# Kernel tuning notes

Hardware: AMD Instinct MI355X
Metric: run time of the kernel (lower is better)

Reference implementation:

```python
import jax, jax.numpy as jnp
import numpy as np

B, L, T = 32, 512, 400
EMB, PRE, ENC, ARNN, DRNN, NSYM = 512, 256, 512, 1024, 1024, 256
MEAN_COEFF, SCALE_COEFF = 1.0, 10.0


def setup_inputs() -> dict:
    key = jax.random.key(0)
    ks = jax.random.split(key, 20)
    s = 0.02
    inp = {
        'memory': jax.random.normal(ks[0], (B, L, ENC), jnp.float32),
        'decoder_inputs': jax.random.normal(ks[1], (B, EMB, T), jnp.float32),
        'memory_lengths': jax.random.randint(ks[2], (B,), L // 2, L + 1).astype(jnp.int64),
        # prenet
        'pW1': jax.random.normal(ks[3], (PRE, EMB), jnp.float32) * s,
        'pb1': jnp.zeros((PRE,), jnp.float32),
        'pW2': jax.random.normal(ks[4], (PRE, PRE), jnp.float32) * s,
        'pb2': jnp.zeros((PRE,), jnp.float32),
        # attention LSTMCell
        'aWih': jax.random.normal(ks[5], (4 * ARNN, PRE + ENC), jnp.float32) * s,
        'aWhh': jax.random.normal(ks[6], (4 * ARNN, ARNN), jnp.float32) * s,
        'abih': jnp.zeros((4 * ARNN,), jnp.float32),
        'abhh': jnp.zeros((4 * ARNN,), jnp.float32),
        # Gaussian attention param linear (weight zero-init in torch; small here)
        'attWp': jax.random.normal(ks[7], (2, ARNN), jnp.float32) * 0.001,
        'attbp': jnp.zeros((2,), jnp.float32),
        # decoder LSTMCell
        'dWih': jax.random.normal(ks[8], (4 * DRNN, ARNN + ENC), jnp.float32) * s,
        'dWhh': jax.random.normal(ks[9], (4 * DRNN, DRNN), jnp.float32) * s,
        'dbih': jnp.zeros((4 * DRNN,), jnp.float32),
        'dbhh': jnp.zeros((4 * DRNN,), jnp.float32),
        # output linear
        'oW': jax.random.normal(ks[10], (NSYM, DRNN + ENC), jnp.float32) * s,
        'ob': jnp.zeros((NSYM,), jnp.float32),
    }
    return inp


def _lstm_cell(x, h, c, Wih, Whh, bih, bhh):
    g = x @ Wih.T + bih + h @ Whh.T + bhh
    i, f, gg, o = jnp.split(g, 4, axis=-1)
    c = jax.nn.sigmoid(f) * c + jax.nn.sigmoid(i) * jnp.tanh(gg)
    h = jax.nn.sigmoid(o) * jnp.tanh(c)
    return h, c


def _decoder_core(memory, decoder_inputs, memory_lengths,
                  pW1, pb1, pW2, pb2,
                  aWih, aWhh, abih, abhh,
                  attWp, attbp,
                  dWih, dWhh, dbih, dbhh,
                  oW, ob):
    b = memory.shape[0]
    Lm = memory.shape[1]
    # go frame + time-major inputs -> prenet (dropout is identity in eval)
    x = jnp.transpose(decoder_inputs, (2, 0, 1))            # [T, B, EMB]
    x = jnp.concatenate([jnp.zeros((1, b, EMB), x.dtype), x], axis=0)  # [T+1, B, EMB]
    x = jax.nn.relu(x @ pW1.T + pb1)
    x = jax.nn.relu(x @ pW2.T + pb2)                        # [T+1, B, PRE]
    x = x[:T]                                               # loop runs T steps

    lin = jnp.arange(Lm, dtype=memory.dtype)[None, :]       # [1, L]
    pad_mask = lin >= memory_lengths[:, None].astype(memory.dtype)  # [B, L] True at pad

    def step(carry, x_t):
        ah, ac, dh, dc, ctx, mean = carry
        cell_in = jnp.concatenate([x_t, ctx], axis=1)
        ah, ac = _lstm_cell(cell_in, ah, ac, aWih, aWhh, abih, abhh)
        params = ah @ attWp.T + attbp                       # [B, 2]
        mean = mean + jnp.exp(params[:, 0:1]) * MEAN_COEFF  # [B, 1]
        scale = jnp.exp(params[:, 1:2]) * SCALE_COEFF       # [B, 1]
        Z = jnp.sqrt(2.0 * np.pi * scale ** 2)
        w = jnp.exp(-0.5 * (lin - mean) ** 2 / scale ** 2) / Z  # [B, L]
        w = jnp.where(pad_mask, 0.0, w)
        ctx = jnp.einsum('bl,bld->bd', w, memory)           # [B, ENC]
        dec_in = jnp.concatenate([ah, ctx], axis=1)
        dh, dc = _lstm_cell(dec_in, dh, dc, dWih, dWhh, dbih, dbhh)
        out = jnp.concatenate([dh, ctx], axis=1) @ oW.T + ob  # [B, NSYM]
        return (ah, ac, dh, dc, ctx, mean), (out, w, params)

    z = jnp.zeros
    carry0 = (z((b, ARNN)), z((b, ARNN)), z((b, DRNN)), z((b, DRNN)),
              z((b, ENC)), z((b, 1)))
    _, (logits, aligns, ps) = jax.lax.scan(step, carry0, x)
    # time-major -> [B, T, ...]
    return (jnp.transpose(logits, (1, 0, 2)),
            jnp.transpose(aligns, (1, 0, 2)),
            jnp.transpose(ps, (1, 0, 2)))


def reference(memory, decoder_inputs, memory_lengths,
              pW1, pb1, pW2, pb2,
              aWih, aWhh, abih, abhh,
              attWp, attbp,
              dWih, dWhh, dbih, dbhh,
              oW, ob):
    return _decoder_core(memory, decoder_inputs, memory_lengths,
                         pW1, pb1, pW2, pb2,
                         aWih, aWhh, abih, abhh,
                         attWp, attbp,
                         dWih, dWhh, dbih, dbhh,
                         oW, ob)
```

## Files before the change

### kernel.cpp

```cpp
#include <hip/hip_runtime.h>
#include <math.h>

#define Bsz   32
#define Lmem  512
#define Tsteps 400
#define EMBD  512
#define PRE   256
#define ENCD  512
#define ARNN  1024
#define DRNN  1024
#define NSYM  256

typedef _Float16 f16x8 __attribute__((ext_vector_type(8)));
typedef float    f32x4 __attribute__((ext_vector_type(4)));
typedef _Float16 half_t;

#define KA  (PRE + ENCD + ARNN)
#define KAQ (KA / 4)
#define NMA (KAQ / 32)
#define KD  (ARNN + ENCD + DRNN)
#define KDQ (KD / 4)
#define NMD (KDQ / 32)
#define LDA_A 1800
#define LDA_D 2568

__device__ __forceinline__ void st_agent_f16(half_t* p, half_t v) {
    __hip_atomic_store((unsigned short*)p, __builtin_bit_cast(unsigned short, v),
                       __ATOMIC_RELAXED, __HIP_MEMORY_SCOPE_AGENT);
}
__device__ __forceinline__ void st_agent_f32(float* p, float v) {
    __hip_atomic_store(p, v, __ATOMIC_RELAXED, __HIP_MEMORY_SCOPE_AGENT);
}
__device__ __forceinline__ void st_agent_u32(unsigned* p, unsigned v) {
    __hip_atomic_store(p, v, __ATOMIC_RELAXED, __HIP_MEMORY_SCOPE_AGENT);
}
__device__ __forceinline__ float ld_agent_f32(const float* p) {
    return __hip_atomic_load(p, __ATOMIC_RELAXED, __HIP_MEMORY_SCOPE_AGENT);
}
__device__ __forceinline__ unsigned ld_agent_u32(const unsigned* p) {
    return __hip_atomic_load(p, __ATOMIC_RELAXED, __HIP_MEMORY_SCOPE_AGENT);
}
__device__ __forceinline__ f16x8 ld_agent_f16x8(const half_t* p) {
    union { unsigned long long u[2]; f16x8 v; } c;
    c.u[0] = __hip_atomic_load((const unsigned long long*)p,
                               __ATOMIC_RELAXED, __HIP_MEMORY_SCOPE_AGENT);
    c.u[1] = __hip_atomic_load(((const unsigned long long*)p) + 1,
                               __ATOMIC_RELAXED, __HIP_MEMORY_SCOPE_AGENT);
    return c.v;
}

template<int KIH, int KHH>
__global__ __launch_bounds__(256) void conv_lstm_w(
    const float* __restrict__ Wih, const float* __restrict__ Whh,
    const float* __restrict__ bih, const float* __restrict__ bhh,
    half_t* __restrict__ Wcat, float* __restrict__ bsum)
{
    constexpr int K = KIH + KHH;
    const int j = blockIdx.x;
    const float* srcA = Wih + (size_t)j * KIH;
    const float* srcB = Whh + (size_t)j * KHH;
    half_t* dst = Wcat + (size_t)j * K;
    for (int k = threadIdx.x; k < KIH; k += 256) dst[k]       = (half_t)srcA[k];
    for (int k = threadIdx.x; k < KHH; k += 256) dst[KIH + k] = (half_t)srcB[k];
    if (threadIdx.x == 0) bsum[j] = bih[j] + bhh[j];
}

__global__ __launch_bounds__(256) void conv_mat(
    const float* __restrict__ src, half_t* __restrict__ dst, int n)
{
    for (int i = blockIdx.x * 256 + threadIdx.x; i < n; i += gridDim.x * 256)
        dst[i] = (half_t)src[i];
}

__global__ __launch_bounds__(256) void prenet_kernel(
    const float* __restrict__ din,
    const float* __restrict__ pW1, const float* __restrict__ pb1,
    const float* __restrict__ pW2, const float* __restrict__ pb2,
    half_t* __restrict__ xpre)
{
    __shared__ float xs[8][EMBD];
    __shared__ float h1s[8][PRE];
    const int tid = threadIdx.x;
    const int row0 = blockIdx.x * 8;

    for (int idx = tid; idx < 8 * EMBD; idx += 256) {
        int r = idx >> 9;
        int e = idx & 511;
        int rid = row0 + r;
        int t = rid >> 5;
        int b = rid & 31;
        float v = 0.f;
        if (t > 0) v = din[(size_t)b * EMBD * Tsteps + (size_t)e * Tsteps + (t - 1)];
        xs[r][e] = v;
    }
    __syncthreads();

    {
        float acc[8] = {0.f,0.f,0.f,0.f,0.f,0.f,0.f,0.f};
        const float* wr = pW1 + (size_t)tid * EMBD;
        for (int e = 0; e < EMBD; e += 4) {
            float4 wv = *(const float4*)(wr + e);
            #pragma unroll
            for (int r = 0; r < 8; ++r) {
                float4 xv = *(const float4*)&xs[r][e];
                acc[r] += wv.x * xv.x + wv.y * xv.y + wv.z * xv.z + wv.w * xv.w;
            }
        }
        float bias = pb1[tid];
        #pragma unroll
        for (int r = 0; r < 8; ++r) h1s[r][tid] = fmaxf(acc[r] + bias, 0.f);
    }
    __syncthreads();

    {
        float acc[8] = {0.f,0.f,0.f,0.f,0.f,0.f,0.f,0.f};
        const float* wr = pW2 + (size_t)tid * PRE;
        for (int e = 0; e < PRE; e += 4) {
            float4 wv = *(const float4*)(wr + e);
            #pragma unroll
            for (int r = 0; r < 8; ++r) {
                float4 xv = *(const float4*)&h1s[r][e];
                acc[r] += wv.x * xv.x + wv.y * xv.y + wv.z * xv.z + wv.w * xv.w;
            }
        }
        float bias = pb2[tid];
        #pragma unroll
        for (int r = 0; r < 8; ++r) {
            int rid = row0 + r;
            int t = rid >> 5;
            int b = rid & 31;
            xpre[(size_t)t * Bsz * PRE + (size_t)b * PRE + tid] =
                (half_t)fmaxf(acc[r] + bias, 0.f);
        }
    }
}

__device__ __forceinline__ void gsync(unsigned* flags, unsigned ph)
{
    asm volatile("s_waitcnt vmcnt(0)" ::: "memory");
    __syncthreads();
    if (threadIdx.x == 0)
        __hip_atomic_store(flags + blockIdx.x * 16, ph,
                           __ATOMIC_RELAXED, __HIP_MEMORY_SCOPE_AGENT);
    if (threadIdx.x < 64) {
        const unsigned* f = flags + threadIdx.x * 64;
        for (;;) {
            unsigned a = ld_agent_u32(f);
            unsigned b = ld_agent_u32(f + 16);
            unsigned c = ld_agent_u32(f + 32);
            unsigned d = ld_agent_u32(f + 48);
            unsigned m = min(min(a, b), min(c, d));
            if (m >= ph) break;
            __builtin_amdgcn_s_sleep(2);
        }
    }
    __syncthreads();
}

__global__ __launch_bounds__(512, 1) void decoder_persistent(
    const half_t* __restrict__ Wcat_a, const float* __restrict__ bsum_a,
    const half_t* __restrict__ Wcat_d, const float* __restrict__ bsum_d,
    const half_t* __restrict__ Wo, const float* __restrict__ ob,
    const half_t* __restrict__ xpre,
    const float* __restrict__ attWp, const float* __restrict__ attbp,
    const int* __restrict__ mlen, const half_t* __restrict__ mem16,
    half_t* __restrict__ ah0, half_t* __restrict__ ah1,
    half_t* __restrict__ dh0, half_t* __restrict__ dh1,
    half_t* __restrict__ ctx0, half_t* __restrict__ ctx1,
    float* __restrict__ mean0, float* __restrict__ mean1,
    float* __restrict__ logits, float* __restrict__ aligns,
    float* __restrict__ ps,
    unsigned* flags)
{
    const int blk   = blockIdx.x;
    const int tid   = threadIdx.x;
    const int wave  = tid >> 6;
    const int lane  = tid & 63;
    const int btile = wave & 1;
    const int kq    = wave >> 1;
    const int m15   = lane & 15;
    const int kh    = lane >> 4;
    const int u0    = blk << 2;
    const int bb    = (btile << 4) + m15;

    __shared__ __align__(16) half_t wAl[16 * LDA_A];
    __shared__ __align__(16) half_t wDl[16 * LDA_D];
    __shared__ float gred[4][2][16][16];
    __shared__ float wsh[Lmem];
    __shared__ float lred[16][33];
    __shared__ float wred8[8][2];
    __shared__ float bc2[2];

    for (int g = tid; g < 16 * (KA / 8); g += 512) {
        int r = g / (KA / 8);
        int c = (g - r * (KA / 8)) * 8;
        int jr = (r >> 2) * 1024 + u0 + (r & 3);
        *(f16x8*)(wAl + r * LDA_A + c) = *(const f16x8*)(Wcat_a + (size_t)jr * KA + c);
    }
    for (int g = tid; g < 16 * (KD / 8); g += 512) {
        int r = g / (KD / 8);
        int c = (g - r * (KD / 8)) * 8;
        int jr = (r >> 2) * 1024 + u0 + (r & 3);
        *(f16x8*)(wDl + r * LDA_D + c) = *(const f16x8*)(Wcat_d + (size_t)jr * KD + c);
    }
    float bsA[4] = {0.f,0.f,0.f,0.f}, bsD[4] = {0.f,0.f,0.f,0.f};
    float cA = 0.f, cD = 0.f;
    if (tid < 128) {
        const int ul = tid >> 5;
        #pragma unroll
        for (int gi = 0; gi < 4; ++gi) {
            bsA[gi] = bsum_a[gi * 1024 + u0 + ul];
            bsD[gi] = bsum_d[gi * 1024 + u0 + ul];
        }
    }
    const half_t* lA = wAl + m15 * LDA_A + kq * KAQ + (kh << 3);
    const half_t* lD = wDl + m15 * LDA_D + kq * KDQ + (kh << 3);
    __syncthreads();

    unsigned ph = 0;

    for (int t = 0; t <= Tsteps; ++t) {
        const int par = t & 1;
        half_t*       ah_cur  = par ? ah1 : ah0;
        const half_t* ah_prv  = par ? ah0 : ah1;
        half_t*       ctx_cur = par ? ctx1 : ctx0;
        const half_t* ctx_prv = par ? ctx0 : ctx1;
        float*        mn_cur  = par ? mean1 : mean0;
        const float*  mn_prv  = par ? mean0 : mean1;
        half_t*       dh_s    = par ? dh0 : dh1;
        const half_t* dh_prv  = par ? dh1 : dh0;

        {
            f16x8 bvA[NMA];
            f16x8 bvD[NMD];
            if (t < Tsteps) {
                const half_t* s0 = xpre + (size_t)t * Bsz * PRE;
                #pragma unroll
                for (int i = 0; i < NMA; ++i) {
                    const int kg = kq * KAQ + i * 32 + (kh << 3);
                    const half_t* bp = (kg < PRE)        ? (s0 + bb * PRE + kg)
                                     : (kg < PRE + ENCD) ? (ctx_prv + bb * ENCD + (kg - PRE))
                                                         : (ah_prv + bb * ARNN + (kg - PRE - ENCD));
                    bvA[i] = ld_agent_f16x8(bp);
                }
            }
            if (t > 0) {
                #pragma unroll
                for (int i = 0; i < NMD; ++i) {
                    const int kg = kq * KDQ + i * 32 + (kh << 3);
                    const half_t* bp = (kg < ARNN)        ? (ah_prv + bb * ARNN + kg)
                                     : (kg < ARNN + ENCD) ? (ctx_prv + bb * ENCD + (kg - ARNN))
                                                          : (dh_prv + bb * DRNN + (kg - ARNN - ENCD));
                    bvD[i] = ld_agent_f16x8(bp);
                }
            }
            if (t < Tsteps) {
                f32x4 accA = {0.f,0.f,0.f,0.f};
                #pragma unroll
                for (int i = 0; i < NMA; ++i) {
                    f16x8 av = *(const f16x8*)(lA + i * 32);
                    accA = __builtin_amdgcn_mfma_f32_16x16x32_f16(av, bvA[i], accA, 0, 0, 0);
                }
                #pragma unroll
                for (int r = 0; r < 4; ++r)
                    gred[kq][btile][(kh << 2) + r][m15] = accA[r];
                __syncthreads();
                if (tid < 128) {
                    const int ul = tid >> 5;
                    const int bq = tid & 31;
                    const int bt = bq >> 4;
                    const int nn = bq & 15;
                    float g[4];
                    #pragma unroll
                    for (int gi = 0; gi < 4; ++gi) {
                        const int mr = (gi << 2) + ul;
                        g[gi] = gred[0][bt][mr][nn] + gred[1][bt][mr][nn]
                              + gred[2][bt][mr][nn] + gred[3][bt][mr][nn] + bsA[gi];
                    }
                    float si = 1.f / (1.f + expf(-g[0]));
                    float sf = 1.f / (1.f + expf(-g[1]));
                    float so = 1.f / (1.f + expf(-g[3]));
                    cA = sf * cA + si * tanhf(g[2]);
                    st_agent_f16(&ah_cur[bq * 1024 + u0 + ul], (half_t)(so * tanhf(cA)));
                }
                __syncthreads();
            }
            if (t > 0) {
                f32x4 accD = {0.f,0.f,0.f,0.f};
                #pragma unroll
                for (int i = 0; i < NMD; ++i) {
                    f16x8 av = *(const f16x8*)(lD + i * 32);
                    accD = __builtin_amdgcn_mfma_f32_16x16x32_f16(av, bvD[i], accD, 0, 0, 0);
                }
                #pragma unroll
                for (int r = 0; r < 4; ++r)
                    gred[kq][btile][(kh << 2) + r][m15] = accD[r];
                __syncthreads();
                if (tid < 128) {
                    const int ul = tid >> 5;
                    const int bq = tid & 31;
                    const int bt = bq >> 4;
                    const int nn = bq & 15;
                    float g[4];
                    #pragma unroll
                    for (int gi = 0; gi < 4; ++gi) {
                        const int mr = (gi << 2) + ul;
                        g[gi] = gred[0][bt][mr][nn] + gred[1][bt][mr][nn]
                              + gred[2][bt][mr][nn] + gred[3][bt][mr][nn] + bsD[gi];
                    }
                    float si = 1.f / (1.f + expf(-g[0]));
                    float sf = 1.f / (1.f + expf(-g[1]));
                    float so = 1.f / (1.f + expf(-g[3]));
                    cD = sf * cD + si * tanhf(g[2]);
                    st_agent_f16(&dh_s[bq * 1024 + u0 + ul], (half_t)(so * tanhf(cD)));
                }
            }
        }
        ++ph; gsync(flags, ph);

        if (t < Tsteps) {
            const int abt = blk >> 3;
            const int dt  = blk & 7;
            float p0, p1;
            {
                union { unsigned u; _Float16 h[2]; } a;
                a.u = ld_agent_u32((const unsigned*)(ah_cur + abt * ARNN + 2 * tid));
                float a0 = (float)a.h[0], a1 = (float)a.h[1];
                float2 w0 = *(const float2*)(attWp + 2 * tid);
                float2 w1 = *(const float2*)(attWp + ARNN + 2 * tid);
                p0 = a0 * w0.x + a1 * w0.y;
                p1 = a0 * w1.x + a1 * w1.y;
            }
            #pragma unroll
            for (int off = 32; off > 0; off >>= 1) {
                p0 += __shfl_down(p0, off, 64);
                p1 += __shfl_down(p1, off, 64);
            }
            if (lane == 0) { wred8[wave][0] = p0; wred8[wave][1] = p1; }
            __syncthreads();
            if (tid == 0) {
                float q0 = attbp[0], q1 = attbp[1];
                #pragma unroll
                for (int w = 0; w < 8; ++w) { q0 += wred8[w][0]; q1 += wred8[w][1]; }
                float mn = ld_agent_f32(&mn_prv[abt]) + expf(q0) * 1.0f;
                float sc = expf(q1) * 10.0f;
                if (dt == 0) {
                    st_agent_f32(&mn_cur[abt], mn);
                    st_agent_f32(&ps[(size_t)abt * Tsteps * 2 + (size_t)t * 2 + 0], q0);
                    st_agent_f32(&ps[(size_t)abt * Tsteps * 2 + (size_t)t * 2 + 1], q1);
                }
                bc2[0] = mn; bc2[1] = sc;
            }
            __syncthreads();
            const float mn = bc2[0], sc = bc2[1];
            const float inv_s = 1.f / sc;
            const float coef = 0.3989422804014327f * inv_s;
            const int len = mlen[abt];
            {
                float z = ((float)tid - mn) * inv_s;
                float wv = (tid < len) ? expf(-0.5f * z * z) * coef : 0.f;
                wsh[tid] = wv;
                if (dt == 0)
                    st_agent_f32(&aligns[(size_t)abt * Tsteps * Lmem + (size_t)t * Lmem + tid], wv);
            }
            __syncthreads();
            int lo = (int)fmaxf(0.f, floorf(mn - 9.f * sc));
            int hi = (int)fminf((float)len, ceilf(mn + 9.f * sc) + 1.f);
            const int d8 = (dt << 6) + (wave << 3);
            const half_t* mb = mem16 + (size_t)abt * Lmem * ENCD + d8;
            float acc[8] = {0.f,0.f,0.f,0.f,0.f,0.f,0.f,0.f};
            for (int l = lo + lane; l < hi; l += 64) {
                f16x8 mv = *(const f16x8*)(mb + (size_t)l * ENCD);
                float w = wsh[l];
                #pragma unroll
                for (int j = 0; j < 8; ++j) acc[j] += w * (float)mv[j];
            }
            #pragma unroll
            for (int off = 32; off > 0; off >>= 1) {
                #pragma unroll
                for (int j = 0; j < 8; ++j) acc[j] += __shfl_down(acc[j], off, 64);
            }
            if (lane == 0) {
                #pragma unroll
                for (int j = 0; j < 4; ++j) {
                    union { unsigned u; _Float16 h[2]; } pk;
                    pk.h[0] = (_Float16)acc[2 * j];
                    pk.h[1] = (_Float16)acc[2 * j + 1];
                    st_agent_u32((unsigned*)(ctx_cur + abt * ENCD + d8 + 2 * j), pk.u);
                }
            }
        }
        if (t > 0) {
            const int b_o = tid & 31;
            const int ks  = tid >> 5;
            const half_t* wrow = Wo + (size_t)blk * (DRNN + ENCD) + ks * 96;
            f16x8 wv[12], av[12];
            #pragma unroll
            for (int c8 = 0; c8 < 12; ++c8) {
                const int k = ks * 96 + c8 * 8;
                wv[c8] = *(const f16x8*)(wrow + c8 * 8);
                const half_t* ap = (k < DRNN) ? (dh_s + b_o * DRNN + k)
                                              : (ctx_prv + b_o * ENCD + (k - DRNN));
                av[c8] = ld_agent_f16x8(ap);
            }
            float outacc = 0.f;
            #pragma unroll
            for (int c8 = 0; c8 < 12; ++c8)
                #pragma unroll
                for (int e = 0; e < 8; ++e)
                    outacc += (float)wv[c8][e] * (float)av[c8][e];
            lred[ks][b_o] = outacc;
            __syncthreads();
            if (tid < 32) {
                float s = 0.f;
                #pragma unroll
                for (int q = 0; q < 16; ++q) s += lred[q][tid];
                st_agent_f32(&logits[(size_t)tid * Tsteps * NSYM + (size_t)(t - 1) * NSYM + blk],
                             s + ob[blk]);
            }
        }
        if (t < Tsteps) { ++ph; gsync(flags, ph); }
    }
}

extern "C" void kernel_launch(void* const* d_in, const int* in_sizes, int n_in,
                              void* d_out, int out_size, void* d_ws, size_t ws_size,
                              hipStream_t stream)
{
    (void)in_sizes; (void)n_in; (void)out_size; (void)ws_size;
    const float* memory = (const float*)d_in[0];
    const float* din    = (const float*)d_in[1];
    const int*   mlen   = (const int*)d_in[2];
    const float* pW1    = (const float*)d_in[3];
    const float* pb1    = (const float*)d_in[4];
    const float* pW2    = (const float*)d_in[5];
    const float* pb2    = (const float*)d_in[6];
    const float* aWih   = (const float*)d_in[7];
    const float* aWhh   = (const float*)d_in[8];
    const float* abih   = (const float*)d_in[9];
    const float* abhh   = (const float*)d_in[10];
    const float* attWp  = (const float*)d_in[11];
    const float* attbp  = (const float*)d_in[12];
    const float* dWih   = (const float*)d_in[13];
    const float* dWhh   = (const float*)d_in[14];
    const float* dbih   = (const float*)d_in[15];
    const float* dbhh   = (const float*)d_in[16];
    const float* oW     = (const float*)d_in[17];
    const float* ob     = (const float*)d_in[18];

    float* logits = (float*)d_out;
    float* aligns = logits + (size_t)Bsz * Tsteps * NSYM;
    float* ps     = aligns + (size_t)Bsz * Tsteps * Lmem;

    char* base = (char*)d_ws;
    auto alloc = [&](size_t bytes) -> char* {
        char* p = base; base += (bytes + 255) & ~(size_t)255; return p;
    };
    half_t* Wcat_a = (half_t*)alloc((size_t)4096 * KA * 2);
    half_t* Wcat_d = (half_t*)alloc((size_t)4096 * KD * 2);
    half_t* Wo     = (half_t*)alloc((size_t)NSYM * (DRNN + ENCD) * 2);
    float*  bsum_a = (float*)alloc(4096 * 4);
    float*  bsum_d = (float*)alloc(4096 * 4);
    half_t* xpre   = (half_t*)alloc((size_t)Tsteps * Bsz * PRE * 2);
    half_t* mem16  = (half_t*)alloc((size_t)Bsz * Lmem * ENCD * 2);
    half_t* ah0    = (half_t*)alloc(Bsz * ARNN * 2);
    half_t* ah1    = (half_t*)alloc(Bsz * ARNN * 2);
    half_t* dh0    = (half_t*)alloc(Bsz * DRNN * 2);
    half_t* dh1    = (half_t*)alloc(Bsz * DRNN * 2);
    half_t* ctx0   = (half_t*)alloc(Bsz * ENCD * 2);
    half_t* ctx1   = (half_t*)alloc(Bsz * ENCD * 2);
    float*  mean0  = (float*)alloc(Bsz * 4);
    float*  mean1  = (float*)alloc(Bsz * 4);
    unsigned* flags = (unsigned*)alloc(256 * 16 * 4);

    (void)hipMemsetAsync(ah1,   0, Bsz * ARNN * 2, stream);
    (void)hipMemsetAsync(dh1,   0, Bsz * DRNN * 2, stream);
    (void)hipMemsetAsync(ctx1,  0, Bsz * ENCD * 2, stream);
    (void)hipMemsetAsync(mean0, 0, Bsz * 4, stream);
    (void)hipMemsetAsync(mean1, 0, Bsz * 4, stream);
    (void)hipMemsetAsync(flags, 0, 256 * 16 * 4, stream);

    conv_lstm_w<PRE + ENCD, ARNN><<<4096, 256, 0, stream>>>(
        aWih, aWhh, abih, abhh, Wcat_a, bsum_a);
    conv_lstm_w<ARNN + ENCD, DRNN><<<4096, 256, 0, stream>>>(
        dWih, dWhh, dbih, dbhh, Wcat_d, bsum_d);
    conv_mat<<<768, 256, 0, stream>>>(oW, Wo, NSYM * (DRNN + ENCD));
    conv_mat<<<4096, 256, 0, stream>>>(memory, mem16, Bsz * Lmem * ENCD);
    prenet_kernel<<<Tsteps * Bsz / 8, 256, 0, stream>>>(din, pW1, pb1, pW2, pb2, xpre);

    decoder_persistent<<<256, 512, 0, stream>>>(
        Wcat_a, bsum_a, Wcat_d, bsum_d, Wo, ob, xpre,
        attWp, attbp, mlen, mem16,
        ah0, ah1, dh0, dh1, ctx0, ctx1, mean0, mean1,
        logits, aligns, ps,
        flags);
}
```

Baseline: 16.26 ms.

## Split grid barrier into arrive/wait and prefetch next-step operands during barrier

```diff
diff --git a/kernel.cpp b/kernel.cpp
--- a/kernel.cpp
+++ b/kernel.cpp
@@ -135,13 +135,16 @@
     }
 }
 
-__device__ __forceinline__ void gsync(unsigned* flags, unsigned ph)
+__device__ __forceinline__ void g_arrive(unsigned* flags, unsigned ph)
 {
     asm volatile("s_waitcnt vmcnt(0)" ::: "memory");
     __syncthreads();
     if (threadIdx.x == 0)
         __hip_atomic_store(flags + blockIdx.x * 16, ph,
                            __ATOMIC_RELAXED, __HIP_MEMORY_SCOPE_AGENT);
+}
+__device__ __forceinline__ void g_wait(unsigned* flags, unsigned ph)
+{
     if (threadIdx.x < 64) {
         const unsigned* f = flags + threadIdx.x * 64;
         for (;;) {
@@ -149,8 +152,7 @@
             unsigned b = ld_agent_u32(f + 16);
             unsigned c = ld_agent_u32(f + 32);
             unsigned d = ld_agent_u32(f + 48);
-            unsigned m = min(min(a, b), min(c, d));
-            if (m >= ph) break;
+            if (min(min(a, b), min(c, d)) >= ph) break;
             __builtin_amdgcn_s_sleep(2);
         }
     }
@@ -185,7 +187,8 @@
 
     __shared__ __align__(16) half_t wAl[16 * LDA_A];
     __shared__ __align__(16) half_t wDl[16 * LDA_D];
-    __shared__ float gred[4][2][16][16];
+    __shared__ float gredA[4][2][16][16];
+    __shared__ float gredD[4][2][16][16];
     __shared__ float wsh[Lmem];
     __shared__ float lred[16][33];
     __shared__ float wred8[8][2];
@@ -208,115 +211,103 @@
     if (tid < 128) {
         const int ul = tid >> 5;
         #pragma unroll
-        for (int gi = 0; gi < 4; ++gi) {
-            bsA[gi] = bsum_a[gi * 1024 + u0 + ul];
-            bsD[gi] = bsum_d[gi * 1024 + u0 + ul];
-        }
+        for (int gi = 0; gi < 4; ++gi) bsA[gi] = bsum_a[gi * 1024 + u0 + ul];
+    } else if (tid < 256) {
+        const int ul = (tid - 128) >> 5;
+        #pragma unroll
+        for (int gi = 0; gi < 4; ++gi) bsD[gi] = bsum_d[gi * 1024 + u0 + ul];
     }
     const half_t* lA = wAl + m15 * LDA_A + kq * KAQ + (kh << 3);
     const half_t* lD = wDl + m15 * LDA_D + kq * KDQ + (kh << 3);
     __syncthreads();
 
+    f16x8 bvA[NMA], bvD[NMD];
+    {
+        const half_t* s0 = xpre;
+        #pragma unroll
+        for (int i = 0; i < NMA; ++i) {
+            const int kg = kq * KAQ + i * 32 + (kh << 3);
+            if (kg < PRE)             bvA[i] = *(const f16x8*)(s0 + bb * PRE + kg);
+            else if (kg < PRE + ENCD) bvA[i] = ld_agent_f16x8(ctx1 + bb * ENCD + (kg - PRE));
+            else                      bvA[i] = ld_agent_f16x8(ah1 + bb * ARNN + (kg - PRE - ENCD));
+        }
+    }
+
     unsigned ph = 0;
 
     for (int t = 0; t <= Tsteps; ++t) {
         const int par = t & 1;
         half_t*       ah_cur  = par ? ah1 : ah0;
-        const half_t* ah_prv  = par ? ah0 : ah1;
         half_t*       ctx_cur = par ? ctx1 : ctx0;
         const half_t* ctx_prv = par ? ctx0 : ctx1;
         float*        mn_cur  = par ? mean1 : mean0;
         const float*  mn_prv  = par ? mean0 : mean1;
         half_t*       dh_s    = par ? dh0 : dh1;
-        const half_t* dh_prv  = par ? dh1 : dh0;
-
-        {
-            f16x8 bvA[NMA];
-            f16x8 bvD[NMD];
+
+        if (t < Tsteps) {
+            f32x4 accA = {0.f,0.f,0.f,0.f};
+            #pragma unroll
+            for (int i = 0; i < NMA; ++i) {
+                f16x8 av = *(const f16x8*)(lA + i * 32);
+                accA = __builtin_amdgcn_mfma_f32_16x16x32_f16(av, bvA[i], accA, 0, 0, 0);
+            }
+            #pragma unroll
+            for (int r = 0; r < 4; ++r)
+                gredA[kq][btile][(kh << 2) + r][m15] = accA[r];
+        }
+        if (t > 0) {
+            f32x4 accD = {0.f,0.f,0.f,0.f};
+            #pragma unroll
+            for (int i = 0; i < NMD; ++i) {
+                f16x8 av = *(const f16x8*)(lD + i * 32);
+                accD = __builtin_amdgcn_mfma_f32_16x16x32_f16(av, bvD[i], accD, 0, 0, 0);
+            }
+            #pragma unroll
+            for (int r = 0; r < 4; ++r)
+                gredD[kq][btile][(kh << 2) + r][m15] = accD[r];
+        }
+        __syncthreads();
+        if (tid < 128) {
             if (t < Tsteps) {
-                const half_t* s0 = xpre + (size_t)t * Bsz * PRE;
-                #pragma unroll
-                for (int i = 0; i < NMA; ++i) {
-                    const int kg = kq * KAQ + i * 32 + (kh << 3);
-                    const half_t* bp = (kg < PRE)        ? (s0 + bb * PRE + kg)
-                                     : (kg < PRE + ENCD) ? (ctx_prv + bb * ENCD + (kg - PRE))
-                                                         : (ah_prv + bb * ARNN + (kg - PRE - ENCD));
-                    bvA[i] = ld_agent_f16x8(bp);
-                }
-            }
+                const int ul = tid >> 5;
+                const int bq = tid & 31;
+                const int bt = bq >> 4;
+                const int nn = bq & 15;
+                float g[4];
+                #pragma unroll
+                for (int gi = 0; gi < 4; ++gi) {
+                    const int mr = (gi << 2) + ul;
+                    g[gi] = gredA[0][bt][mr][nn] + gredA[1][bt][mr][nn]
+                          + gredA[2][bt][mr][nn] + gredA[3][bt][mr][nn] + bsA[gi];
+                }
+                float si = 1.f / (1.f + expf(-g[0]));
+                float sf = 1.f / (1.f + expf(-g[1]));
+                float so = 1.f / (1.f + expf(-g[3]));
+                cA = sf * cA + si * tanhf(g[2]);
+                st_agent_f16(&ah_cur[bq * 1024 + u0 + ul], (half_t)(so * tanhf(cA)));
+            }
+        } else if (tid < 256) {
             if (t > 0) {
-                #pragma unroll
-                for (int i = 0; i < NMD; ++i) {
-                    const int kg = kq * KDQ + i * 32 + (kh << 3);
-                    const half_t* bp = (kg < ARNN)        ? (ah_prv + bb * ARNN + kg)
-                                     : (kg < ARNN + ENCD) ? (ctx_prv + bb * ENCD + (kg - ARNN))
-                                                          : (dh_prv + bb * DRNN + (kg - ARNN - ENCD));
-                    bvD[i] = ld_agent_f16x8(bp);
-                }
-            }
-            if (t < Tsteps) {
-                f32x4 accA = {0.f,0.f,0.f,0.f};
-                #pragma unroll
-                for (int i = 0; i < NMA; ++i) {
-                    f16x8 av = *(const f16x8*)(lA + i * 32);
-                    accA = __builtin_amdgcn_mfma_f32_16x16x32_f16(av, bvA[i], accA, 0, 0, 0);
-                }
-                #pragma unroll
-                for (int r = 0; r < 4; ++r)
-                    gred[kq][btile][(kh << 2) + r][m15] = accA[r];
-                __syncthreads();
-                if (tid < 128) {
-                    const int ul = tid >> 5;
-                    const int bq = tid & 31;
-                    const int bt = bq >> 4;
-                    const int nn = bq & 15;
-                    float g[4];
-                    #pragma unroll
-                    for (int gi = 0; gi < 4; ++gi) {
-                        const int mr = (gi << 2) + ul;
-                        g[gi] = gred[0][bt][mr][nn] + gred[1][bt][mr][nn]
-                              + gred[2][bt][mr][nn] + gred[3][bt][mr][nn] + bsA[gi];
-                    }
-                    float si = 1.f / (1.f + expf(-g[0]));
-                    float sf = 1.f / (1.f + expf(-g[1]));
-                    float so = 1.f / (1.f + expf(-g[3]));
-                    cA = sf * cA + si * tanhf(g[2]);
-                    st_agent_f16(&ah_cur[bq * 1024 + u0 + ul], (half_t)(so * tanhf(cA)));
-                }
-                __syncthreads();
-            }
-            if (t > 0) {
-                f32x4 accD = {0.f,0.f,0.f,0.f};
-                #pragma unroll
-                for (int i = 0; i < NMD; ++i) {
-                    f16x8 av = *(const f16x8*)(lD + i * 32);
-                    accD = __builtin_amdgcn_mfma_f32_16x16x32_f16(av, bvD[i], accD, 0, 0, 0);
-                }
-                #pragma unroll
-                for (int r = 0; r < 4; ++r)
-                    gred[kq][btile][(kh << 2) + r][m15] = accD[r];
-                __syncthreads();
-                if (tid < 128) {
-                    const int ul = tid >> 5;
-                    const int bq = tid & 31;
-                    const int bt = bq >> 4;
-                    const int nn = bq & 15;
-                    float g[4];
-                    #pragma unroll
-                    for (int gi = 0; gi < 4; ++gi) {
-                        const int mr = (gi << 2) + ul;
-                        g[gi] = gred[0][bt][mr][nn] + gred[1][bt][mr][nn]
-                              + gred[2][bt][mr][nn] + gred[3][bt][mr][nn] + bsD[gi];
-                    }
-                    float si = 1.f / (1.f + expf(-g[0]));
-                    float sf = 1.f / (1.f + expf(-g[1]));
-                    float so = 1.f / (1.f + expf(-g[3]));
-                    cD = sf * cD + si * tanhf(g[2]);
-                    st_agent_f16(&dh_s[bq * 1024 + u0 + ul], (half_t)(so * tanhf(cD)));
-                }
-            }
-        }
-        ++ph; gsync(flags, ph);
+                const int lt = tid - 128;
+                const int ul = lt >> 5;
+                const int bq = lt & 31;
+                const int bt = bq >> 4;
+                const int nn = bq & 15;
+                float g[4];
+                #pragma unroll
+                for (int gi = 0; gi < 4; ++gi) {
+                    const int mr = (gi << 2) + ul;
+                    g[gi] = gredD[0][bt][mr][nn] + gredD[1][bt][mr][nn]
+                          + gredD[2][bt][mr][nn] + gredD[3][bt][mr][nn] + bsD[gi];
+                }
+                float si = 1.f / (1.f + expf(-g[0]));
+                float sf = 1.f / (1.f + expf(-g[1]));
+                float so = 1.f / (1.f + expf(-g[3]));
+                cD = sf * cD + si * tanhf(g[2]);
+                st_agent_f16(&dh_s[bq * 1024 + u0 + ul], (half_t)(so * tanhf(cD)));
+            }
+        }
+        ++ph; g_arrive(flags, ph); g_wait(flags, ph);
 
         if (t < Tsteps) {
             const int abt = blk >> 3;
@@ -394,21 +385,25 @@
             const int b_o = tid & 31;
             const int ks  = tid >> 5;
             const half_t* wrow = Wo + (size_t)blk * (DRNN + ENCD) + ks * 96;
-            f16x8 wv[12], av[12];
-            #pragma unroll
-            for (int c8 = 0; c8 < 12; ++c8) {
-                const int k = ks * 96 + c8 * 8;
-                wv[c8] = *(const f16x8*)(wrow + c8 * 8);
-                const half_t* ap = (k < DRNN) ? (dh_s + b_o * DRNN + k)
-                                              : (ctx_prv + b_o * ENCD + (k - DRNN));
-                av[c8] = ld_agent_f16x8(ap);
-            }
             float outacc = 0.f;
             #pragma unroll
-            for (int c8 = 0; c8 < 12; ++c8)
-                #pragma unroll
-                for (int e = 0; e < 8; ++e)
-                    outacc += (float)wv[c8][e] * (float)av[c8][e];
+            for (int half = 0; half < 2; ++half) {
+                f16x8 wv[6], av[6];
+                #pragma unroll
+                for (int c8 = 0; c8 < 6; ++c8) {
+                    const int cc = half * 6 + c8;
+                    const int k = ks * 96 + cc * 8;
+                    wv[c8] = *(const f16x8*)(wrow + cc * 8);
+                    const half_t* ap = (k < DRNN) ? (dh_s + b_o * DRNN + k)
+                                                  : (ctx_prv + b_o * ENCD + (k - DRNN));
+                    av[c8] = ld_agent_f16x8(ap);
+                }
+                #pragma unroll
+                for (int c8 = 0; c8 < 6; ++c8)
+                    #pragma unroll
+                    for (int e = 0; e < 8; ++e)
+                        outacc += (float)wv[c8][e] * (float)av[c8][e];
+            }
             lred[ks][b_o] = outacc;
             __syncthreads();
             if (tid < 32) {
@@ -419,7 +414,43 @@
                              s + ob[blk]);
             }
         }
-        if (t < Tsteps) { ++ph; gsync(flags, ph); }
+        if (t < Tsteps) {
+            ++ph; g_arrive(flags, ph);
+            if (t + 1 < Tsteps) {
+                const half_t* s0n = xpre + (size_t)(t + 1) * Bsz * PRE;
+                #pragma unroll
+                for (int i = 0; i < NMA; ++i) {
+                    const int kg = kq * KAQ + i * 32 + (kh << 3);
+                    if (kg < PRE)
+                        bvA[i] = *(const f16x8*)(s0n + bb * PRE + kg);
+                    else if (kg >= PRE + ENCD)
+                        bvA[i] = ld_agent_f16x8(ah_cur + bb * ARNN + (kg - PRE - ENCD));
+                }
+            }
+            #pragma unroll
+            for (int i = 0; i < NMD; ++i) {
+                const int kg = kq * KDQ + i * 32 + (kh << 3);
+                if (kg < ARNN)
+                    bvD[i] = ld_agent_f16x8(ah_cur + bb * ARNN + kg);
+                else if (kg >= ARNN + ENCD)
+                    bvD[i] = ld_agent_f16x8(dh_s + bb * DRNN + (kg - ARNN - ENCD));
+            }
+            g_wait(flags, ph);
+            if (t + 1 < Tsteps) {
+                #pragma unroll
+                for (int i = 0; i < NMA; ++i) {
+                    const int kg = kq * KAQ + i * 32 + (kh << 3);
+                    if (kg >= PRE && kg < PRE + ENCD)
+                        bvA[i] = ld_agent_f16x8(ctx_cur + bb * ENCD + (kg - PRE));
+                }
+            }
+            #pragma unroll
+            for (int i = 0; i < NMD; ++i) {
+                const int kg = kq * KDQ + i * 32 + (kh << 3);
+                if (kg >= ARNN && kg < ARNN + ENCD)
+                    bvD[i] = ld_agent_f16x8(ctx_cur + bb * ENCD + (kg - ARNN));
+            }
+        }
     }
 }
 
```

New measurement: 14.29 ms. -12.1%, faster.
